# Kernel optimization log

Hardware: AMD Instinct MI355X
Metric: run time of the kernel (lower is better)

The kernel has to match this reference:

```python
import jax, jax.numpy as jnp
import numpy as np


def _mlp1(x, W, b):
    return jax.nn.relu(x @ W + b)


def _forward(battle_x, side_x, user_x, moveset_feat, movepool_feat, lookup_move_feat,
             lookup_move_mask, lastberry, lastberry_mask, items, abilities, types_x,
             tera_types_x, opt_moves, move_mask, can_tera, switch_mask,
             W_item, b_item, W_ab, b_ab, W_ms, b_ms, W_user, b_user,
             W_mo1, b_mo1, W_mo2, b_mo2, W_so1, b_so1, W_so2, b_so2,
             active_idx, switch_idx):
    B = battle_x.shape[0]
    # --- user block (vectorized over [B, 2 sides, 6 team members]) ---
    ms = _mlp1(moveset_feat, W_ms, b_ms)                    # [B,2,6,4,128]
    pool = _mlp1(movepool_feat, W_ms, b_ms).mean(axis=-2)   # [B,2,6,128] mean over move pool
    move_set_x = jnp.maximum(ms.max(axis=-2), pool)         # max over [4 slots + pool-mean]
    item_x = _mlp1(items, W_item, b_item).mean(axis=-2)     # [B,2,6,128]
    ability_x = _mlp1(abilities, W_ab, b_ab).mean(axis=-2)  # [B,2,6,128]
    # optional lookup slots: mask*relu(Wx+b) == zero vector when absent
    lk = _mlp1(lookup_move_feat, W_ms, b_ms) * lookup_move_mask[..., None]  # [B,2,6,5,128]
    berry = _mlp1(lastberry, W_item, b_item) * lastberry_mask[..., None]    # [B,2,6,128]
    lk_flat = lk.reshape(B, 2, 6, 5 * 128)
    u_in = jnp.concatenate([user_x, lk_flat, berry, move_set_x, item_x, ability_x,
                            types_x, tera_types_x], axis=-1)                # [B,2,6,1281]
    u = _mlp1(u_in, W_user, b_user)                                         # [B,2,6,512]
    # --- side block ---
    active = jnp.take_along_axis(u, active_idx[:, :, None, None], axis=2)[:, :, 0]  # [B,2,512]
    side_out = jnp.concatenate([side_x, active, u.max(axis=2)], axis=-1)    # [B,2,1041]
    battle_full = jnp.concatenate([battle_x, side_out[:, 0], side_out[:, 1]], axis=-1)  # [B,2091]
    D = battle_full.shape[-1]
    # --- move options: 4 moves x tera in {0,1} ---
    bt = jnp.broadcast_to(battle_full[:, None, None, :], (B, 4, 2, D))
    mv = jnp.broadcast_to(opt_moves[:, :, None, :], (B, 4, 2, 128))
    tera = jnp.broadcast_to(jnp.arange(2, dtype=battle_x.dtype)[None, None, :, None], (B, 4, 2, 1))
    xm = jnp.concatenate([bt, mv, tera], axis=-1)                           # [B,4,2,2220]
    mlogit = (_mlp1(xm, W_mo1, b_mo1) @ W_mo2 + b_mo2)[..., 0]              # [B,4,2]
    tera_ok = jnp.stack([jnp.ones_like(can_tera), can_tera], axis=-1)       # [B,2]
    mvalid = move_mask[:, :, None] * tera_ok[:, None, :]
    mlogit = jnp.where(mvalid > 0, mlogit, -jnp.inf).reshape(B, 8)
    # --- switch options ---
    sw = jnp.take_along_axis(u[:, 0], switch_idx[:, :, None], axis=1)       # [B,6,512]
    xs = jnp.concatenate([jnp.broadcast_to(battle_full[:, None, :], (B, 6, D)), sw], axis=-1)
    slogit = (_mlp1(xs, W_so1, b_so1) @ W_so2 + b_so2)[..., 0]              # [B,6]
    slogit = jnp.where(switch_mask > 0, slogit, -jnp.inf)
    return jnp.concatenate([mlogit, slogit], axis=-1)                       # [B,14]


def setup_inputs() -> dict:
    key = jax.random.key(0)
    ks = jax.random.split(key, 40)
    B = 512
    f32 = jnp.float32
    n = lambda k, s, sc=1.0: jax.random.normal(k, s, f32) * sc
    bern = lambda k, s, p: (jax.random.uniform(k, s) < p).astype(f32)
    inp = {
        'battle_x': n(ks[0], (B, 9)),
        'side_x': n(ks[1], (B, 2, 17)),
        'user_x': n(ks[2], (B, 2, 6, 89)),
        'moveset_feat': n(ks[3], (B, 2, 6, 4, 516)),
        'movepool_feat': n(ks[4], (B, 2, 6, 8, 516)),
        'lookup_move_feat': n(ks[5], (B, 2, 6, 5, 516)),
        'lookup_move_mask': bern(ks[6], (B, 2, 6, 5), 0.5),
        'lastberry': n(ks[7], (B, 2, 6, 256)),
        'lastberry_mask': bern(ks[8], (B, 2, 6), 0.5),
        'items': n(ks[9], (B, 2, 6, 2, 256)),
        'abilities': n(ks[10], (B, 2, 6, 2, 256)),
        'types_x': bern(ks[11], (B, 2, 6, 20), 0.1),
        'tera_types_x': bern(ks[12], (B, 2, 6, 20), 0.1),
        'opt_moves': n(ks[13], (B, 4, 128)),
        'move_mask': bern(ks[14], (B, 4), 0.9),
        'can_tera': bern(ks[15], (B,), 0.5),
        'switch_mask': bern(ks[16], (B, 6), 0.8),
        'W_item': n(ks[17], (256, 128), 0.05), 'b_item': n(ks[18], (128,), 0.05),
        'W_ab': n(ks[19], (256, 128), 0.05), 'b_ab': n(ks[20], (128,), 0.05),
        'W_ms': n(ks[21], (516, 128), 0.05), 'b_ms': n(ks[22], (128,), 0.05),
        'W_user': n(ks[23], (1281, 512), 0.02), 'b_user': n(ks[24], (512,), 0.02),
        'W_mo1': n(ks[25], (2220, 512), 0.02), 'b_mo1': n(ks[26], (512,), 0.02),
        'W_mo2': n(ks[27], (512, 1), 0.05), 'b_mo2': n(ks[28], (1,), 0.05),
        'W_so1': n(ks[29], (2603, 512), 0.02), 'b_so1': n(ks[30], (512,), 0.02),
        'W_so2': n(ks[31], (512, 1), 0.05), 'b_so2': n(ks[32], (1,), 0.05),
        'active_idx': jax.random.randint(ks[33], (B, 2), 0, 6),
        'switch_idx': jax.random.randint(ks[34], (B, 6), 0, 6),
    }
    return inp


def reference(battle_x, side_x, user_x, moveset_feat, movepool_feat, lookup_move_feat,
              lookup_move_mask, lastberry, lastberry_mask, items, abilities, types_x,
              tera_types_x, opt_moves, move_mask, can_tera, switch_mask,
              W_item, b_item, W_ab, b_ab, W_ms, b_ms, W_user, b_user,
              W_mo1, b_mo1, W_mo2, b_mo2, W_so1, b_so1, W_so2, b_so2,
              active_idx, switch_idx):
    return _forward(battle_x, side_x, user_x, moveset_feat, movepool_feat, lookup_move_feat,
                    lookup_move_mask, lastberry, lastberry_mask, items, abilities, types_x,
                    tera_types_x, opt_moves, move_mask, can_tera, switch_mask,
                    W_item, b_item, W_ab, b_ab, W_ms, b_ms, W_user, b_user,
                    W_mo1, b_mo1, W_mo2, b_mo2, W_so1, b_so1, W_so2, b_so2,
                    active_idx, switch_idx)
```

## Files before the change

kernel.cpp:

```cpp
#include <hip/hip_runtime.h>
#include <math.h>

#define BATCH 512
#define NEG_BIG (-3.0e38f)

typedef __attribute__((ext_vector_type(8))) short short8;
typedef __attribute__((ext_vector_type(4))) float floatx4;

__device__ inline unsigned pk2(float lo, float hi) {
    return __builtin_amdgcn_perm(__float_as_uint(hi), __float_as_uint(lo), 0x07060302u);
}
__device__ inline short8 cvt8(float4 a, float4 b) {
    union { unsigned u[4]; short8 s; } r;
    r.u[0] = pk2(a.x, a.y); r.u[1] = pk2(a.z, a.w);
    r.u[2] = pk2(b.x, b.y); r.u[3] = pk2(b.z, b.w);
    return r.s;
}
__device__ inline short f2bf(float f) {
    unsigned u = __float_as_uint(f);
    u += 0x7FFFu + ((u >> 16) & 1u);
    return (short)(u >> 16);
}
__device__ inline float bf2f(short s) {
    return __uint_as_float(((unsigned)(unsigned short)s) << 16);
}

__device__ inline void wprep_body(
    const float* __restrict__ W, int K, int N,
    short* __restrict__ Wt, int KP, int k_off,
    int lid, int kbt, float (*tile)[33])
{
    const int kb = (lid % kbt) * 32, nb = (lid / kbt) * 32;
    const int c = threadIdx.x & 31, r0 = threadIdx.x >> 5;
    #pragma unroll
    for (int i = 0; i < 4; ++i) {
        const int r = r0 + i * 8;
        const int k = kb + r;
        tile[r][c] = (k < K) ? W[(size_t)k * N + nb + c] : 0.f;
    }
    __syncthreads();
    #pragma unroll
    for (int i = 0; i < 4; ++i) {
        const int n = nb + r0 + i * 8;
        Wt[(size_t)n * KP + k_off + kb + c] = f2bf(tile[c][r0 + i * 8]);
    }
}

__global__ __launch_bounds__(256) void k_wprep_all(
    const float* __restrict__ W_ms, const float* __restrict__ W_item,
    const float* __restrict__ W_ab, const float* __restrict__ W_user,
    const float* __restrict__ W_mo1, const float* __restrict__ W_so1,
    short* __restrict__ Wt_pre, short* __restrict__ Wt_user,
    short* __restrict__ Wt_mo, short* __restrict__ Wt_mv,
    short* __restrict__ Wt_so, short* __restrict__ Wt_sw)
{
    __shared__ float tile[32][33];
    const int l = blockIdx.x;
    if      (l < 68)   wprep_body(W_ms,   516,  128, Wt_pre,  1056, 0,   l,        17, tile);
    else if (l < 100)  wprep_body(W_item, 256,  128, Wt_pre,  1056, 544, l - 68,   8,  tile);
    else if (l < 132)  wprep_body(W_ab,   256,  128, Wt_pre,  1056, 800, l - 100,  8,  tile);
    else if (l < 788)  wprep_body(W_user, 1281, 512, Wt_user, 1312, 0,   l - 132,  41, tile);
    else if (l < 1844) wprep_body(W_mo1,  2091, 512, Wt_mo,   2112, 0,   l - 788,  66, tile);
    else if (l < 1908) wprep_body(W_mo1 + (size_t)2091 * 512, 128, 512, Wt_mv, 128, 0, l - 1844, 4, tile);
    else if (l < 2964) wprep_body(W_so1,  2091, 512, Wt_so,   2112, 0,   l - 1908, 66, tile);
    else               wprep_body(W_so1 + (size_t)2091 * 512, 512, 512, Wt_sw, 512, 0, l - 2964, 16, tile);
}

#define STRA 552
#define SIOFF 18768
#define STRI 264
#define ZEROE 528

__device__ inline void stage4(short* S, int e, float4 v) {
    uint2 wv; wv.x = pk2(v.x, v.y); wv.y = pk2(v.z, v.w);
    *(uint2*)(S + e) = wv;
}

__global__ __launch_bounds__(256) void k_pre_gemm(
    const float* __restrict__ moveset, const float* __restrict__ movepool,
    const float* __restrict__ lookup,  const float* __restrict__ items,
    const float* __restrict__ lastberry, const float* __restrict__ abilities,
    const float* __restrict__ lookup_mask, const float* __restrict__ berry_mask,
    const float* __restrict__ user_x, const float* __restrict__ types_x,
    const float* __restrict__ tera_types,
    const short* __restrict__ Wt,
    const float* __restrict__ b_ms, const float* __restrict__ b_item,
    const float* __restrict__ b_ab,
    short* __restrict__ u_in)
{
    __shared__ __align__(16) short S[21408];
    const int t = threadIdx.x;
    const int bsu0 = blockIdx.x * 2;

    {
        const float4* msrc = (const float4*)(moveset + (size_t)bsu0 * 4 * 516);
        for (int i = t; i < 1032; i += 256) {
            const int g = i / 129, j = i - g * 129;
            stage4(S, ((g >> 2) * 17 + (g & 3)) * STRA + j * 4, msrc[i]);
        }
        const float4* psrc = (const float4*)(movepool + (size_t)bsu0 * 8 * 516);
        for (int i = t; i < 2064; i += 256) {
            const int g = i / 129, j = i - g * 129;
            stage4(S, ((g >> 3) * 17 + 4 + (g & 7)) * STRA + j * 4, psrc[i]);
        }
        const float4* lsrc = (const float4*)(lookup + (size_t)bsu0 * 5 * 516);
        for (int i = t; i < 1290; i += 256) {
            const int g = i / 129, j = i - g * 129;
            const int b = g / 5, r = g - b * 5;
            stage4(S, (b * 17 + 12 + r) * STRA + j * 4, lsrc[i]);
        }
        const float4* isrc = (const float4*)(items + (size_t)bsu0 * 2 * 256);
        for (int i = t; i < 256; i += 256) {
            const int g = i >> 6, j = i & 63;
            stage4(S, SIOFF + ((g >> 1) * 5 + (g & 1)) * STRI + j * 4, isrc[i]);
        }
        const float4* bsrc = (const float4*)(lastberry + (size_t)bsu0 * 256);
        for (int i = t; i < 128; i += 256) {
            const int g = i >> 6, j = i & 63;
            stage4(S, SIOFF + (g * 5 + 2) * STRI + j * 4, bsrc[i]);
        }
        const float4* asrc = (const float4*)(abilities + (size_t)bsu0 * 2 * 256);
        for (int i = t; i < 256; i += 256) {
            const int g = i >> 6, j = i & 63;
            stage4(S, SIOFF + ((g >> 1) * 5 + 3 + (g & 1)) * STRI + j * 4, asrc[i]);
        }
        for (int i = t; i < 476; i += 256) {
            const int rr = i / 14, p = i - rr * 14;
            *(unsigned*)(S + rr * STRA + 516 + p * 2) = 0u;
        }
    }
    __syncthreads();

    const int lane = t & 63, w = t >> 6;
    const int m = lane & 15, q = lane >> 4;

    int t2base = ZEROE, t2lo = 1, t2hi = 0;
    {
        int jj = m, b = 0;
        if (m >= 6 && m < 12) { b = 1; jj = m - 6; }
        if (m < 12) {
            if (jj == 0)      { t2base = (b * 17 + 16) * STRA;             t2lo = 0;  t2hi = 16; }
            else if (jj <= 2) { t2base = SIOFF + (b * 5 + (jj - 1)) * STRI; t2lo = 17; t2hi = 24; }
            else if (jj == 3) { t2base = SIOFF + (b * 5 + 2) * STRI;        t2lo = 17; t2hi = 24; }
            else              { t2base = SIOFF + (b * 5 + 3 + (jj - 4)) * STRI; t2lo = 25; t2hi = 32; }
        }
    }
    const short* bp0 = Wt + (size_t)(w * 32 + m) * 1056 + q * 8;
    const short* bp1 = bp0 + (size_t)16 * 1056;

    floatx4 acc[3][2];
    #pragma unroll
    for (int i = 0; i < 3; ++i) {
        acc[i][0] = (floatx4){0.f, 0.f, 0.f, 0.f};
        acc[i][1] = (floatx4){0.f, 0.f, 0.f, 0.f};
    }

    short8 Bc0 = *(const short8*)bp0;
    short8 Bc1 = *(const short8*)bp1;
    const int aoff = q * 8;

    for (int s = 0; s <= 16; ++s) {
        short8 Bn0 = *(const short8*)(bp0 + (s + 1) * 32);
        short8 Bn1 = *(const short8*)(bp1 + (s + 1) * 32);
        const int k0 = s * 32 + aoff;
        short8 a0 = *(const short8*)(S + m * STRA + k0);
        short8 a1 = *(const short8*)(S + (17 + m) * STRA + k0);
        const int e2 = (s >= t2lo && s <= t2hi) ? t2base + (s - t2lo) * 32 + aoff : ZEROE;
        short8 a2 = *(const short8*)(S + e2);
        acc[0][0] = __builtin_amdgcn_mfma_f32_16x16x32_bf16(a0, Bc0, acc[0][0], 0, 0, 0);
        acc[0][1] = __builtin_amdgcn_mfma_f32_16x16x32_bf16(a0, Bc1, acc[0][1], 0, 0, 0);
        acc[1][0] = __builtin_amdgcn_mfma_f32_16x16x32_bf16(a1, Bc0, acc[1][0], 0, 0, 0);
        acc[1][1] = __builtin_amdgcn_mfma_f32_16x16x32_bf16(a1, Bc1, acc[1][1], 0, 0, 0);
        acc[2][0] = __builtin_amdgcn_mfma_f32_16x16x32_bf16(a2, Bc0, acc[2][0], 0, 0, 0);
        acc[2][1] = __builtin_amdgcn_mfma_f32_16x16x32_bf16(a2, Bc1, acc[2][1], 0, 0, 0);
        Bc0 = Bn0; Bc1 = Bn1;
    }
    for (int s = 17; s <= 32; ++s) {
        const int sn = (s + 1 > 32) ? 32 : s + 1;
        short8 Bn0 = *(const short8*)(bp0 + sn * 32);
        short8 Bn1 = *(const short8*)(bp1 + sn * 32);
        const int e2 = (s >= t2lo && s <= t2hi) ? t2base + (s - t2lo) * 32 + aoff : ZEROE;
        short8 a2 = *(const short8*)(S + e2);
        acc[2][0] = __builtin_amdgcn_mfma_f32_16x16x32_bf16(a2, Bc0, acc[2][0], 0, 0, 0);
        acc[2][1] = __builtin_amdgcn_mfma_f32_16x16x32_bf16(a2, Bc1, acc[2][1], 0, 0, 0);
        Bc0 = Bn0; Bc1 = Bn1;
    }

    __syncthreads();
    float* ec = (float*)S;

    #pragma unroll
    for (int nt = 0; nt < 2; ++nt) {
        const int col = w * 32 + nt * 16 + m;
        #pragma unroll
        for (int r = 0; r < 4; ++r) {
            const int row = q * 4 + r;
            ec[col * 49 + row]      = acc[0][nt][r];
            ec[col * 49 + 24 + row] = acc[1][nt][r];
            if (row < 6)            ec[col * 49 + 16 + row]            = acc[2][nt][r];
            else if (row < 12)      ec[col * 49 + 24 + 16 + (row - 6)] = acc[2][nt][r];
        }
    }
    __syncthreads();
    {
        const int c  = t & 127;
        const int bi = t >> 7;
        const int bsu = bsu0 + bi;
        const float* v = &ec[c * 49 + bi * 24];
        short* __restrict__ orow = u_in + (size_t)bsu * 1312;
        const float bms = b_ms[c], bit = b_item[c], bab = b_ab[c];
        float msx = 0.f;
        #pragma unroll
        for (int r = 0; r < 4; ++r) msx = fmaxf(msx, v[r] + bms);
        float pool = 0.f;
        #pragma unroll
        for (int r = 4; r < 12; ++r) pool += fmaxf(v[r] + bms, 0.f);
        pool *= 0.125f;
        orow[857 + c] = f2bf(fmaxf(msx, pool));
        #pragma unroll
        for (int sl = 0; sl < 5; ++sl) {
            const float mask = lookup_mask[bsu * 5 + sl];
            orow[89 + sl * 128 + c] = f2bf(fmaxf(v[12 + sl] + bms, 0.f) * mask);
        }
        orow[985 + c]  = f2bf(0.5f * (fmaxf(v[17] + bit, 0.f) + fmaxf(v[18] + bit, 0.f)));
        orow[729 + c]  = f2bf(fmaxf(v[19] + bit, 0.f) * berry_mask[bsu]);
        orow[1113 + c] = f2bf(0.5f * (fmaxf(v[20] + bab, 0.f) + fmaxf(v[21] + bab, 0.f)));
        if (c < 89) orow[c] = f2bf(user_x[(size_t)bsu * 89 + c]);
        if (c < 20) {
            orow[1241 + c] = f2bf(types_x[bsu * 20 + c]);
            orow[1261 + c] = f2bf(tera_types[bsu * 20 + c]);
        }
        if (c < 31) orow[1281 + c] = 0;
    }
}

template<int AMODE, bool ABF16, bool RELU, bool HASBIAS, bool OBF16>
__global__ __launch_bounds__(256, 3) void k_gemm(
    const void* __restrict__ Av, int strideA,
    const void* __restrict__ gbasev, const int* __restrict__ gidx,
    const short* __restrict__ Wt, int KP,
    const float* __restrict__ bias,
    void* __restrict__ Cv, size_t partStride, int ksteps)
{
    const int t = threadIdx.x, lane = t & 63, w = t >> 6;
    const int m = lane & 15, q = lane >> 4;
    const int mb = blockIdx.x * 64;
    const int nb = blockIdx.y * 128 + w * 32;
    const int z = blockIdx.z;
    const int koff = z * ksteps * 32;

    const short* aps[4]; const float* apf[4];
    #pragma unroll
    for (int i = 0; i < 4; ++i) {
        const int row = mb + i * 16 + m;
        size_t roff;
        if (AMODE == 0) roff = (size_t)row * strideA;
        else {
            const int bb = row / 6, j = row - bb * 6;
            roff = ((size_t)bb * 12 + gidx[bb * 6 + j]) * 512;
        }
        if (ABF16) aps[i] = (const short*)Av + roff + koff + q * 8;
        else       apf[i] = (const float*)Av + roff + koff + q * 8;
        if (AMODE == 1) aps[i] = (const short*)gbasev + roff + koff + q * 8;
    }
    const short* bp0 = Wt + (size_t)(nb + m) * KP + koff + q * 8;
    const short* bp1 = bp0 + (size_t)16 * KP;

    floatx4 acc[4][2];
    #pragma unroll
    for (int i = 0; i < 4; ++i) {
        acc[i][0] = (floatx4){0.f, 0.f, 0.f, 0.f};
        acc[i][1] = (floatx4){0.f, 0.f, 0.f, 0.f};
    }

    short8 Acur[4]; short8 Bc0, Bc1;
    #pragma unroll
    for (int i = 0; i < 4; ++i) {
        if (ABF16) Acur[i] = *(const short8*)(aps[i]);
        else       Acur[i] = cvt8(*(const float4*)(apf[i]), *(const float4*)(apf[i] + 4));
    }
    Bc0 = *(const short8*)bp0;
    Bc1 = *(const short8*)bp1;

    for (int s = 0; s < ksteps - 1; ++s) {
        short8 An[4], Bn0, Bn1;
        const int o = (s + 1) * 32;
        #pragma unroll
        for (int i = 0; i < 4; ++i) {
            if (ABF16) An[i] = *(const short8*)(aps[i] + o);
            else       An[i] = cvt8(*(const float4*)(apf[i] + o), *(const float4*)(apf[i] + o + 4));
        }
        Bn0 = *(const short8*)(bp0 + o);
        Bn1 = *(const short8*)(bp1 + o);
        #pragma unroll
        for (int i = 0; i < 4; ++i) {
            acc[i][0] = __builtin_amdgcn_mfma_f32_16x16x32_bf16(Acur[i], Bc0, acc[i][0], 0, 0, 0);
            acc[i][1] = __builtin_amdgcn_mfma_f32_16x16x32_bf16(Acur[i], Bc1, acc[i][1], 0, 0, 0);
        }
        #pragma unroll
        for (int i = 0; i < 4; ++i) Acur[i] = An[i];
        Bc0 = Bn0; Bc1 = Bn1;
    }
    #pragma unroll
    for (int i = 0; i < 4; ++i) {
        acc[i][0] = __builtin_amdgcn_mfma_f32_16x16x32_bf16(Acur[i], Bc0, acc[i][0], 0, 0, 0);
        acc[i][1] = __builtin_amdgcn_mfma_f32_16x16x32_bf16(Acur[i], Bc1, acc[i][1], 0, 0, 0);
    }

    const float bb0 = (HASBIAS && z == 0) ? bias[nb + m] : 0.f;
    const float bb1 = (HASBIAS && z == 0) ? bias[nb + 16 + m] : 0.f;
    #pragma unroll
    for (int i = 0; i < 4; ++i) {
        #pragma unroll
        for (int r = 0; r < 4; ++r) {
            const int row = mb + i * 16 + q * 4 + r;
            float v0 = acc[i][0][r] + bb0;
            float v1 = acc[i][1][r] + bb1;
            if (RELU) { v0 = fmaxf(v0, 0.f); v1 = fmaxf(v1, 0.f); }
            if (OBF16) {
                short* C = (short*)Cv + z * partStride;
                C[(size_t)row * 512 + nb + m]      = f2bf(v0);
                C[(size_t)row * 512 + nb + 16 + m] = f2bf(v1);
            } else {
                float* C = (float*)Cv + z * partStride;
                C[(size_t)row * 512 + nb + m]      = v0;
                C[(size_t)row * 512 + nb + 16 + m] = v1;
            }
        }
    }
}

__global__ __launch_bounds__(256) void k_battle(
    const float* __restrict__ battle_x, const float* __restrict__ side_x,
    const short* __restrict__ u, const int* __restrict__ active_idx,
    short* __restrict__ bfb)
{
    const int b = blockIdx.x;
    const int t = threadIdx.x;
    short* __restrict__ o = bfb + (size_t)b * 2112;
    if (t < 9) o[t] = f2bf(battle_x[b * 9 + t]);
    if (t < 21) o[2091 + t] = 0;
    for (int s = 0; s < 2; ++s) {
        const short* __restrict__ us = u + (size_t)(b * 2 + s) * 6 * 512;
        const int act = active_idx[b * 2 + s];
        if (t < 17) o[9 + s * 1041 + t] = f2bf(side_x[(b * 2 + s) * 17 + t]);
        for (int c = t; c < 512; c += 256) {
            float mx = bf2f(us[c]);
            #pragma unroll
            for (int uu = 1; uu < 6; ++uu) mx = fmaxf(mx, bf2f(us[uu * 512 + c]));
            o[9 + s * 1041 + 17 + c]       = us[act * 512 + c];
            o[9 + s * 1041 + 17 + 512 + c] = f2bf(mx);
        }
    }
}

__global__ __launch_bounds__(512) void k_epi_mo(
    const float* __restrict__ C_mo, size_t partStride, int nparts,
    const float* __restrict__ D_mv,
    const float* __restrict__ W1, const float* __restrict__ W2,
    const float* __restrict__ b2,
    const float* __restrict__ move_mask, const float* __restrict__ can_tera,
    float* __restrict__ out)
{
    __shared__ float red[8][8];
    const int b = blockIdx.x, t = threadIdx.x;
    float h = 0.f;
    for (int p = 0; p < nparts; ++p) h += C_mo[p * partStride + (size_t)b * 512 + t];
    const float wt = W1[(size_t)2219 * 512 + t];
    const float w2 = W2[t];
    float dm[4];
    #pragma unroll
    for (int m = 0; m < 4; ++m) dm[m] = D_mv[((size_t)b * 4 + m) * 512 + t];
    const int lane = t & 63, wid = t >> 6;
    #pragma unroll
    for (int m = 0; m < 4; ++m) {
        #pragma unroll
        for (int tt = 0; tt < 2; ++tt) {
            float hv = fmaxf(h + dm[m] + (tt ? wt : 0.f), 0.f);
            float v = hv * w2;
            #pragma unroll
            for (int off = 32; off > 0; off >>= 1) v += __shfl_down(v, off);
            if (lane == 0) red[m * 2 + tt][wid] = v;
        }
    }
    __syncthreads();
    if (t < 8) {
        float s = 0.f;
        #pragma unroll
        for (int ww = 0; ww < 8; ++ww) s += red[t][ww];
        s += b2[0];
        const int m = t >> 1, tt = t & 1;
        const float ok = move_mask[b * 4 + m] * (tt ? can_tera[b] : 1.f);
        out[b * 14 + t] = (ok > 0.f) ? s : NEG_BIG;
    }
}

__global__ __launch_bounds__(512) void k_epi_sw(
    const float* __restrict__ C_so, size_t partStride, int nparts,
    const float* __restrict__ D_sw,
    const float* __restrict__ W2, const float* __restrict__ b2,
    const float* __restrict__ switch_mask, float* __restrict__ out)
{
    __shared__ float red[6][8];
    const int b = blockIdx.x, t = threadIdx.x;
    float h = 0.f;
    for (int p = 0; p < nparts; ++p) h += C_so[p * partStride + (size_t)b * 512 + t];
    const float w2 = W2[t];
    const int lane = t & 63, wid = t >> 6;
    #pragma unroll
    for (int j = 0; j < 6; ++j) {
        float hv = fmaxf(h + D_sw[((size_t)b * 6 + j) * 512 + t], 0.f);
        float v = hv * w2;
        #pragma unroll
        for (int off = 32; off > 0; off >>= 1) v += __shfl_down(v, off);
        if (lane == 0) red[j][wid] = v;
    }
    __syncthreads();
    if (t < 6) {
        float s = 0.f;
        #pragma unroll
        for (int ww = 0; ww < 8; ++ww) s += red[t][ww];
        s += b2[0];
        out[b * 14 + 8 + t] = (switch_mask[b * 6 + t] > 0.f) ? s : NEG_BIG;
    }
}

extern "C" void kernel_launch(void* const* d_in, const int* in_sizes, int n_in,
                              void* d_out, int out_size, void* d_ws, size_t ws_size,
                              hipStream_t stream) {
    const float* battle_x    = (const float*)d_in[0];
    const float* side_x      = (const float*)d_in[1];
    const float* user_x      = (const float*)d_in[2];
    const float* moveset     = (const float*)d_in[3];
    const float* movepool    = (const float*)d_in[4];
    const float* lookup      = (const float*)d_in[5];
    const float* lookup_mask = (const float*)d_in[6];
    const float* lastberry   = (const float*)d_in[7];
    const float* berry_mask  = (const float*)d_in[8];
    const float* items       = (const float*)d_in[9];
    const float* abilities   = (const float*)d_in[10];
    const float* types_x     = (const float*)d_in[11];
    const float* tera_types  = (const float*)d_in[12];
    const float* opt_moves   = (const float*)d_in[13];
    const float* move_mask   = (const float*)d_in[14];
    const float* can_tera    = (const float*)d_in[15];
    const float* switch_mask = (const float*)d_in[16];
    const float* W_item = (const float*)d_in[17];
    const float* b_item = (const float*)d_in[18];
    const float* W_ab   = (const float*)d_in[19];
    const float* b_ab   = (const float*)d_in[20];
    const float* W_ms   = (const float*)d_in[21];
    const float* b_ms   = (const float*)d_in[22];
    const float* W_user = (const float*)d_in[23];
    const float* b_user = (const float*)d_in[24];
    const float* W_mo1  = (const float*)d_in[25];
    const float* b_mo1  = (const float*)d_in[26];
    const float* W_mo2  = (const float*)d_in[27];
    const float* b_mo2  = (const float*)d_in[28];
    const float* W_so1  = (const float*)d_in[29];
    const float* b_so1  = (const float*)d_in[30];
    const float* W_so2  = (const float*)d_in[31];
    const float* b_so2  = (const float*)d_in[32];
    const int* active_idx = (const int*)d_in[33];
    const int* switch_idx = (const int*)d_in[34];
    float* out = (float*)d_out;

    char* base = (char*)d_ws;
    size_t off = 0;
    short* u_in = (short*)(base + off); off += (size_t)6144 * 1312 * 2;
    short* u    = (short*)(base + off); off += (size_t)6144 * 512 * 2;
    short* bfb  = (short*)(base + off); off += (size_t)512 * 2112 * 2;
    float* C_mo = (float*)(base + off); off += (size_t)6 * 512 * 512 * 4;
    float* C_so = (float*)(base + off); off += (size_t)6 * 512 * 512 * 4;
    float* D_mv = (float*)(base + off); off += (size_t)2048 * 512 * 4;
    float* D_sw = (float*)(base + off); off += (size_t)3072 * 512 * 4;
    short* Wt_pre  = (short*)(base + off); off += (size_t)128 * 1056 * 2;
    short* Wt_user = (short*)(base + off); off += (size_t)512 * 1312 * 2;
    short* Wt_mo   = (short*)(base + off); off += (size_t)512 * 2112 * 2;
    short* Wt_so   = (short*)(base + off); off += (size_t)512 * 2112 * 2;
    short* Wt_mv   = (short*)(base + off); off += (size_t)512 * 128 * 2;
    short* Wt_sw   = (short*)(base + off); off += (size_t)512 * 512 * 2;

    k_wprep_all<<<3220, 256, 0, stream>>>(W_ms, W_item, W_ab, W_user, W_mo1, W_so1,
                                          Wt_pre, Wt_user, Wt_mo, Wt_mv, Wt_so, Wt_sw);

    k_pre_gemm<<<3072, 256, 0, stream>>>(moveset, movepool, lookup, items, lastberry,
                                         abilities, lookup_mask, berry_mask,
                                         user_x, types_x, tera_types,
                                         Wt_pre, b_ms, b_item, b_ab, u_in);
    k_gemm<0, true, true, true, true><<<dim3(96, 4, 1), 256, 0, stream>>>(
        u_in, 1312, nullptr, nullptr, Wt_user, 1312, b_user, u, 0, 41);
    k_battle<<<BATCH, 256, 0, stream>>>(battle_x, side_x, u, active_idx, bfb);
    k_gemm<0, true, false, true, false><<<dim3(8, 4, 6), 256, 0, stream>>>(
        bfb, 2112, nullptr, nullptr, Wt_mo, 2112, b_mo1, C_mo, (size_t)512 * 512, 11);
    k_gemm<0, false, false, false, false><<<dim3(32, 4, 1), 256, 0, stream>>>(
        opt_moves, 128, nullptr, nullptr, Wt_mv, 128, nullptr, D_mv, 0, 4);
    k_gemm<0, true, false, true, false><<<dim3(8, 4, 6), 256, 0, stream>>>(
        bfb, 2112, nullptr, nullptr, Wt_so, 2112, b_so1, C_so, (size_t)512 * 512, 11);
    k_gemm<1, true, false, false, false><<<dim3(48, 4, 1), 256, 0, stream>>>(
        nullptr, 0, u, switch_idx, Wt_sw, 512, nullptr, D_sw, 0, 16);
    k_epi_mo<<<BATCH, 512, 0, stream>>>(C_mo, (size_t)512 * 512, 6, D_mv, W_mo1,
                                        W_mo2, b_mo2, move_mask, can_tera, out);
    k_epi_sw<<<BATCH, 512, 0, stream>>>(C_so, (size_t)512 * 512, 6, D_sw,
                                        W_so2, b_so2, switch_mask, out);
}
```

Baseline: 491.0 us.

## Deepen load prefetching in pre-GEMM and GEMM kernels, halve GEMM row tile

The pre-GEMM staging now issues all global loads into registers before writing them to shared memory, and adds an occupancy hint of three blocks per CU. Its B-operand loads now use a 4-deep register ring buffer. The generic GEMM drops from 64 to 32 rows per block with grids doubled to match, and prefetches A and B four k-steps ahead instead of one. The aim is to hide global-memory latency and give more blocks to the GPU, at the cost of more registers and less B reuse per block.

```diff
diff --git a/kernel.cpp b/kernel.cpp
--- a/kernel.cpp
+++ b/kernel.cpp
@@ -76,7 +76,7 @@
     *(uint2*)(S + e) = wv;
 }
 
-__global__ __launch_bounds__(256) void k_pre_gemm(
+__global__ __launch_bounds__(256, 3) void k_pre_gemm(
     const float* __restrict__ moveset, const float* __restrict__ movepool,
     const float* __restrict__ lookup,  const float* __restrict__ items,
     const float* __restrict__ lastberry, const float* __restrict__ abilities,
@@ -94,39 +94,70 @@
 
     {
         const float4* msrc = (const float4*)(moveset + (size_t)bsu0 * 4 * 516);
-        for (int i = t; i < 1032; i += 256) {
-            const int g = i / 129, j = i - g * 129;
-            stage4(S, ((g >> 2) * 17 + (g & 3)) * STRA + j * 4, msrc[i]);
-        }
         const float4* psrc = (const float4*)(movepool + (size_t)bsu0 * 8 * 516);
-        for (int i = t; i < 2064; i += 256) {
-            const int g = i / 129, j = i - g * 129;
-            stage4(S, ((g >> 3) * 17 + 4 + (g & 7)) * STRA + j * 4, psrc[i]);
-        }
         const float4* lsrc = (const float4*)(lookup + (size_t)bsu0 * 5 * 516);
-        for (int i = t; i < 1290; i += 256) {
-            const int g = i / 129, j = i - g * 129;
+        const float4* isrc = (const float4*)(items + (size_t)bsu0 * 2 * 256);
+        const float4* bsrc = (const float4*)(lastberry + (size_t)bsu0 * 256);
+        const float4* asrc = (const float4*)(abilities + (size_t)bsu0 * 2 * 256);
+
+        float4 rm[5], rp[9], rl[6], rit, rlb, rab;
+        #pragma unroll
+        for (int j = 0; j < 5; ++j) {
+            int i = t + j * 256; if (i > 1031) i = 1031;
+            rm[j] = msrc[i];
+        }
+        #pragma unroll
+        for (int j = 0; j < 9; ++j) {
+            int i = t + j * 256; if (i > 2063) i = 2063;
+            rp[j] = psrc[i];
+        }
+        #pragma unroll
+        for (int j = 0; j < 6; ++j) {
+            int i = t + j * 256; if (i > 1289) i = 1289;
+            rl[j] = lsrc[i];
+        }
+        rit = isrc[t];
+        rlb = bsrc[t & 127];
+        rab = asrc[t];
+
+        #pragma unroll
+        for (int j = 0; j < 5; ++j) {
+            int i = t + j * 256; if (i > 1031) i = 1031;
+            const int g = i / 129, jj = i - g * 129;
+            stage4(S, ((g >> 2) * 17 + (g & 3)) * STRA + jj * 4, rm[j]);
+        }
+        #pragma unroll
+        for (int j = 0; j < 9; ++j) {
+            int i = t + j * 256; if (i > 2063) i = 2063;
+            const int g = i / 129, jj = i - g * 129;
+            stage4(S, ((g >> 3) * 17 + 4 + (g & 7)) * STRA + jj * 4, rp[j]);
+        }
+        #pragma unroll
+        for (int j = 0; j < 6; ++j) {
+            int i = t + j * 256; if (i > 1289) i = 1289;
+            const int g = i / 129, jj = i - g * 129;
             const int b = g / 5, r = g - b * 5;
-            stage4(S, (b * 17 + 12 + r) * STRA + j * 4, lsrc[i]);
-        }
-        const float4* isrc = (const float4*)(items + (size_t)bsu0 * 2 * 256);
-        for (int i = t; i < 256; i += 256) {
-            const int g = i >> 6, j = i & 63;
-            stage4(S, SIOFF + ((g >> 1) * 5 + (g & 1)) * STRI + j * 4, isrc[i]);
-        }
-        const float4* bsrc = (const float4*)(lastberry + (size_t)bsu0 * 256);
-        for (int i = t; i < 128; i += 256) {
-            const int g = i >> 6, j = i & 63;
-            stage4(S, SIOFF + (g * 5 + 2) * STRI + j * 4, bsrc[i]);
-        }
-        const float4* asrc = (const float4*)(abilities + (size_t)bsu0 * 2 * 256);
-        for (int i = t; i < 256; i += 256) {
-            const int g = i >> 6, j = i & 63;
-            stage4(S, SIOFF + ((g >> 1) * 5 + 3 + (g & 1)) * STRI + j * 4, asrc[i]);
-        }
-        for (int i = t; i < 476; i += 256) {
-            const int rr = i / 14, p = i - rr * 14;
-            *(unsigned*)(S + rr * STRA + 516 + p * 2) = 0u;
+            stage4(S, (b * 17 + 12 + r) * STRA + jj * 4, rl[j]);
+        }
+        {
+            const int g = t >> 6, j = t & 63;
+            stage4(S, SIOFF + ((g >> 1) * 5 + (g & 1)) * STRI + j * 4, rit);
+        }
+        {
+            const int i = t & 127, g = i >> 6, j = i & 63;
+            stage4(S, SIOFF + (g * 5 + 2) * STRI + j * 4, rlb);
+        }
+        {
+            const int g = t >> 6, j = t & 63;
+            stage4(S, SIOFF + ((g >> 1) * 5 + 3 + (g & 1)) * STRI + j * 4, rab);
+        }
+        #pragma unroll
+        for (int j = 0; j < 2; ++j) {
+            const int i = t + j * 256;
+            if (i < 476) {
+                const int rr = i / 14, p = i - rr * 14;
+                *(unsigned*)(S + rr * STRA + 516 + p * 2) = 0u;
+            }
         }
     }
     __syncthreads();
@@ -155,35 +186,42 @@
         acc[i][1] = (floatx4){0.f, 0.f, 0.f, 0.f};
     }
 
-    short8 Bc0 = *(const short8*)bp0;
-    short8 Bc1 = *(const short8*)bp1;
+    short8 B0[4], B1[4];
+    #pragma unroll
+    for (int d = 0; d < 4; ++d) {
+        B0[d] = *(const short8*)(bp0 + d * 32);
+        B1[d] = *(const short8*)(bp1 + d * 32);
+    }
     const int aoff = q * 8;
 
+    #pragma unroll
     for (int s = 0; s <= 16; ++s) {
-        short8 Bn0 = *(const short8*)(bp0 + (s + 1) * 32);
-        short8 Bn1 = *(const short8*)(bp1 + (s + 1) * 32);
         const int k0 = s * 32 + aoff;
         short8 a0 = *(const short8*)(S + m * STRA + k0);
         short8 a1 = *(const short8*)(S + (17 + m) * STRA + k0);
         const int e2 = (s >= t2lo && s <= t2hi) ? t2base + (s - t2lo) * 32 + aoff : ZEROE;
         short8 a2 = *(const short8*)(S + e2);
-        acc[0][0] = __builtin_amdgcn_mfma_f32_16x16x32_bf16(a0, Bc0, acc[0][0], 0, 0, 0);
-        acc[0][1] = __builtin_amdgcn_mfma_f32_16x16x32_bf16(a0, Bc1, acc[0][1], 0, 0, 0);
-        acc[1][0] = __builtin_amdgcn_mfma_f32_16x16x32_bf16(a1, Bc0, acc[1][0], 0, 0, 0);
-        acc[1][1] = __builtin_amdgcn_mfma_f32_16x16x32_bf16(a1, Bc1, acc[1][1], 0, 0, 0);
-        acc[2][0] = __builtin_amdgcn_mfma_f32_16x16x32_bf16(a2, Bc0, acc[2][0], 0, 0, 0);
-        acc[2][1] = __builtin_amdgcn_mfma_f32_16x16x32_bf16(a2, Bc1, acc[2][1], 0, 0, 0);
-        Bc0 = Bn0; Bc1 = Bn1;
-    }
+        acc[0][0] = __builtin_amdgcn_mfma_f32_16x16x32_bf16(a0, B0[s & 3], acc[0][0], 0, 0, 0);
+        acc[0][1] = __builtin_amdgcn_mfma_f32_16x16x32_bf16(a0, B1[s & 3], acc[0][1], 0, 0, 0);
+        acc[1][0] = __builtin_amdgcn_mfma_f32_16x16x32_bf16(a1, B0[s & 3], acc[1][0], 0, 0, 0);
+        acc[1][1] = __builtin_amdgcn_mfma_f32_16x16x32_bf16(a1, B1[s & 3], acc[1][1], 0, 0, 0);
+        acc[2][0] = __builtin_amdgcn_mfma_f32_16x16x32_bf16(a2, B0[s & 3], acc[2][0], 0, 0, 0);
+        acc[2][1] = __builtin_amdgcn_mfma_f32_16x16x32_bf16(a2, B1[s & 3], acc[2][1], 0, 0, 0);
+        if (s + 4 <= 32) {
+            B0[s & 3] = *(const short8*)(bp0 + (s + 4) * 32);
+            B1[s & 3] = *(const short8*)(bp1 + (s + 4) * 32);
+        }
+    }
+    #pragma unroll
     for (int s = 17; s <= 32; ++s) {
-        const int sn = (s + 1 > 32) ? 32 : s + 1;
-        short8 Bn0 = *(const short8*)(bp0 + sn * 32);
-        short8 Bn1 = *(const short8*)(bp1 + sn * 32);
         const int e2 = (s >= t2lo && s <= t2hi) ? t2base + (s - t2lo) * 32 + aoff : ZEROE;
         short8 a2 = *(const short8*)(S + e2);
-        acc[2][0] = __builtin_amdgcn_mfma_f32_16x16x32_bf16(a2, Bc0, acc[2][0], 0, 0, 0);
-        acc[2][1] = __builtin_amdgcn_mfma_f32_16x16x32_bf16(a2, Bc1, acc[2][1], 0, 0, 0);
-        Bc0 = Bn0; Bc1 = Bn1;
+        acc[2][0] = __builtin_amdgcn_mfma_f32_16x16x32_bf16(a2, B0[s & 3], acc[2][0], 0, 0, 0);
+        acc[2][1] = __builtin_amdgcn_mfma_f32_16x16x32_bf16(a2, B1[s & 3], acc[2][1], 0, 0, 0);
+        if (s + 4 <= 32) {
+            B0[s & 3] = *(const short8*)(bp0 + (s + 4) * 32);
+            B1[s & 3] = *(const short8*)(bp1 + (s + 4) * 32);
+        }
     }
 
     __syncthreads();
@@ -244,14 +282,14 @@
 {
     const int t = threadIdx.x, lane = t & 63, w = t >> 6;
     const int m = lane & 15, q = lane >> 4;
-    const int mb = blockIdx.x * 64;
+    const int mb = blockIdx.x * 32;
     const int nb = blockIdx.y * 128 + w * 32;
     const int z = blockIdx.z;
     const int koff = z * ksteps * 32;
 
-    const short* aps[4]; const float* apf[4];
-    #pragma unroll
-    for (int i = 0; i < 4; ++i) {
+    const short* aps[2]; const float* apf[2];
+    #pragma unroll
+    for (int i = 0; i < 2; ++i) {
         const int row = mb + i * 16 + m;
         size_t roff;
         if (AMODE == 0) roff = (size_t)row * strideA;
@@ -266,51 +304,70 @@
     const short* bp0 = Wt + (size_t)(nb + m) * KP + koff + q * 8;
     const short* bp1 = bp0 + (size_t)16 * KP;
 
-    floatx4 acc[4][2];
-    #pragma unroll
-    for (int i = 0; i < 4; ++i) {
+    floatx4 acc[2][2];
+    #pragma unroll
+    for (int i = 0; i < 2; ++i) {
         acc[i][0] = (floatx4){0.f, 0.f, 0.f, 0.f};
         acc[i][1] = (floatx4){0.f, 0.f, 0.f, 0.f};
     }
 
-    short8 Acur[4]; short8 Bc0, Bc1;
-    #pragma unroll
-    for (int i = 0; i < 4; ++i) {
-        if (ABF16) Acur[i] = *(const short8*)(aps[i]);
-        else       Acur[i] = cvt8(*(const float4*)(apf[i]), *(const float4*)(apf[i] + 4));
-    }
-    Bc0 = *(const short8*)bp0;
-    Bc1 = *(const short8*)bp1;
-
-    for (int s = 0; s < ksteps - 1; ++s) {
-        short8 An[4], Bn0, Bn1;
-        const int o = (s + 1) * 32;
-        #pragma unroll
-        for (int i = 0; i < 4; ++i) {
-            if (ABF16) An[i] = *(const short8*)(aps[i] + o);
-            else       An[i] = cvt8(*(const float4*)(apf[i] + o), *(const float4*)(apf[i] + o + 4));
-        }
-        Bn0 = *(const short8*)(bp0 + o);
-        Bn1 = *(const short8*)(bp1 + o);
-        #pragma unroll
-        for (int i = 0; i < 4; ++i) {
-            acc[i][0] = __builtin_amdgcn_mfma_f32_16x16x32_bf16(Acur[i], Bc0, acc[i][0], 0, 0, 0);
-            acc[i][1] = __builtin_amdgcn_mfma_f32_16x16x32_bf16(Acur[i], Bc1, acc[i][1], 0, 0, 0);
-        }
-        #pragma unroll
-        for (int i = 0; i < 4; ++i) Acur[i] = An[i];
-        Bc0 = Bn0; Bc1 = Bn1;
-    }
-    #pragma unroll
-    for (int i = 0; i < 4; ++i) {
-        acc[i][0] = __builtin_amdgcn_mfma_f32_16x16x32_bf16(Acur[i], Bc0, acc[i][0], 0, 0, 0);
-        acc[i][1] = __builtin_amdgcn_mfma_f32_16x16x32_bf16(Acur[i], Bc1, acc[i][1], 0, 0, 0);
+    short8 Ab[4][2];
+    float4 Af[4][2][2];
+    short8 B0b[4], B1b[4];
+    #pragma unroll
+    for (int d = 0; d < 4; ++d) {
+        #pragma unroll
+        for (int i = 0; i < 2; ++i) {
+            if (ABF16) Ab[d][i] = *(const short8*)(aps[i] + d * 32);
+            else {
+                Af[d][i][0] = *(const float4*)(apf[i] + d * 32);
+                Af[d][i][1] = *(const float4*)(apf[i] + d * 32 + 4);
+            }
+        }
+        B0b[d] = *(const short8*)(bp0 + d * 32);
+        B1b[d] = *(const short8*)(bp1 + d * 32);
+    }
+
+    int s = 0;
+    for (; s + 4 < ksteps; s += 4) {
+        #pragma unroll
+        for (int d = 0; d < 4; ++d) {
+            #pragma unroll
+            for (int i = 0; i < 2; ++i) {
+                const short8 av = ABF16 ? Ab[d][i] : cvt8(Af[d][i][0], Af[d][i][1]);
+                acc[i][0] = __builtin_amdgcn_mfma_f32_16x16x32_bf16(av, B0b[d], acc[i][0], 0, 0, 0);
+                acc[i][1] = __builtin_amdgcn_mfma_f32_16x16x32_bf16(av, B1b[d], acc[i][1], 0, 0, 0);
+            }
+            int ns = s + d + 4; if (ns > ksteps - 1) ns = ksteps - 1;
+            const int o = ns * 32;
+            #pragma unroll
+            for (int i = 0; i < 2; ++i) {
+                if (ABF16) Ab[d][i] = *(const short8*)(aps[i] + o);
+                else {
+                    Af[d][i][0] = *(const float4*)(apf[i] + o);
+                    Af[d][i][1] = *(const float4*)(apf[i] + o + 4);
+                }
+            }
+            B0b[d] = *(const short8*)(bp0 + o);
+            B1b[d] = *(const short8*)(bp1 + o);
+        }
+    }
+    #pragma unroll
+    for (int d = 0; d < 4; ++d) {
+        if (s + d < ksteps) {
+            #pragma unroll
+            for (int i = 0; i < 2; ++i) {
+                const short8 av = ABF16 ? Ab[d][i] : cvt8(Af[d][i][0], Af[d][i][1]);
+                acc[i][0] = __builtin_amdgcn_mfma_f32_16x16x32_bf16(av, B0b[d], acc[i][0], 0, 0, 0);
+                acc[i][1] = __builtin_amdgcn_mfma_f32_16x16x32_bf16(av, B1b[d], acc[i][1], 0, 0, 0);
+            }
+        }
     }
 
     const float bb0 = (HASBIAS && z == 0) ? bias[nb + m] : 0.f;
     const float bb1 = (HASBIAS && z == 0) ? bias[nb + 16 + m] : 0.f;
     #pragma unroll
-    for (int i = 0; i < 4; ++i) {
+    for (int i = 0; i < 2; ++i) {
         #pragma unroll
         for (int r = 0; r < 4; ++r) {
             const int row = mb + i * 16 + q * 4 + r;
@@ -488,16 +545,16 @@
                                          abilities, lookup_mask, berry_mask,
                                          user_x, types_x, tera_types,
                                          Wt_pre, b_ms, b_item, b_ab, u_in);
-    k_gemm<0, true, true, true, true><<<dim3(96, 4, 1), 256, 0, stream>>>(
+    k_gemm<0, true, true, true, true><<<dim3(192, 4, 1), 256, 0, stream>>>(
         u_in, 1312, nullptr, nullptr, Wt_user, 1312, b_user, u, 0, 41);
     k_battle<<<BATCH, 256, 0, stream>>>(battle_x, side_x, u, active_idx, bfb);
-    k_gemm<0, true, false, true, false><<<dim3(8, 4, 6), 256, 0, stream>>>(
+    k_gemm<0, true, false, true, false><<<dim3(16, 4, 6), 256, 0, stream>>>(
         bfb, 2112, nullptr, nullptr, Wt_mo, 2112, b_mo1, C_mo, (size_t)512 * 512, 11);
-    k_gemm<0, false, false, false, false><<<dim3(32, 4, 1), 256, 0, stream>>>(
+    k_gemm<0, false, false, false, false><<<dim3(64, 4, 1), 256, 0, stream>>>(
         opt_moves, 128, nullptr, nullptr, Wt_mv, 128, nullptr, D_mv, 0, 4);
-    k_gemm<0, true, false, true, false><<<dim3(8, 4, 6), 256, 0, stream>>>(
+    k_gemm<0, true, false, true, false><<<dim3(16, 4, 6), 256, 0, stream>>>(
         bfb, 2112, nullptr, nullptr, Wt_so, 2112, b_so1, C_so, (size_t)512 * 512, 11);
-    k_gemm<1, true, false, false, false><<<dim3(48, 4, 1), 256, 0, stream>>>(
+    k_gemm<1, true, false, false, false><<<dim3(96, 4, 1), 256, 0, stream>>>(
         nullptr, 0, u, switch_idx, Wt_sw, 512, nullptr, D_sw, 0, 16);
     k_epi_mo<<<BATCH, 512, 0, stream>>>(C_mo, (size_t)512 * 512, 6, D_mv, W_mo1,
                                         W_mo2, b_mo2, move_mask, can_tera, out);
```

Result: faster. 470.4 us (-4.2%).
